# Performance work log

Hardware: AMD Instinct MI355X
Metric: run time of the kernel (lower is better)

Reference implementation:

```python
import jax, jax.numpy as jnp
import numpy as np

# ---- hash-grid config (from module source) ----
L = 16          # n_levels
F = 2           # n_features_per_level
T = 1 << 19     # hashmap size
BASE = 16
SCALE = 1.3819
RES = [int(np.floor(BASE * SCALE ** l)) for l in range(L)]
DENSE = [(r + 1) ** 3 <= T for r in RES]   # levels 0-4 dense, rest hashed
PRIMES = np.array([1, 2654435761, 805459861], dtype=np.uint32)
OFFS = np.array([[i, j, k] for k in (0, 1) for j in (0, 1) for i in (0, 1)], dtype=np.float32)  # [8,3]
OFFS_U = OFFS.astype(np.uint32)


def hash_grid_encode(xyz, table):
    # xyz: [N,3] in [0,1); table: [L,T,F]
    feats = []
    for l in range(L):
        res = RES[l]
        pos = xyz * res                      # [N,3]
        p0f = jnp.floor(pos)
        w = pos - p0f                        # trilinear weights, [N,3]
        p0 = p0f.astype(jnp.uint32)          # [N,3]
        corner = p0[:, None, :] + OFFS_U[None]            # [N,8,3] uint32
        if DENSE[l]:
            s = np.uint32(res + 1)
            idx = corner[..., 0] + corner[..., 1] * s + corner[..., 2] * (s * s)
        else:
            idx = (corner[..., 0] * PRIMES[0]) ^ (corner[..., 1] * PRIMES[1]) ^ (corner[..., 2] * PRIMES[2])
            idx = idx % np.uint32(T)
        # corner weights: prod_d (offs ? w : 1-w)  -> [N,8]
        wts = jnp.prod(jnp.where(OFFS[None].astype(bool), w[:, None, :], 1.0 - w[:, None, :]), axis=-1)
        f = table[l][idx]                    # gather: [N,8,F]
        feats.append(jnp.sum(f * wts[..., None], axis=1))  # [N,F]
    return jnp.concatenate(feats, axis=-1)   # [N, L*F=32]


def sh_deg4(d):
    # d in [-1,1]^3; returns [N,16] real SH basis (tcnn ordering/constants)
    x, y, z = d[:, 0], d[:, 1], d[:, 2]
    x2, y2, z2 = x * x, y * y, z * z
    xy, yz, xz = x * y, y * z, x * z
    return jnp.stack([
        jnp.full_like(x, 0.28209479177387814),
        -0.48860251190291987 * y,
        0.48860251190291987 * z,
        -0.48860251190291987 * x,
        1.0925484305920792 * xy,
        -1.0925484305920792 * yz,
        0.94617469575755997 * z2 - 0.31539156525251999,
        -1.0925484305920792 * xz,
        0.54627421529603959 * (x2 - y2),
        0.59004358992664352 * y * (-3.0 * x2 + y2),
        2.8906114426405538 * xy * z,
        0.45704579946446572 * y * (1.0 - 5.0 * z2),
        0.3731763325901154 * z * (5.0 * z2 - 3.0),
        0.45704579946446572 * x * (1.0 - 5.0 * z2),
        1.4453057213202769 * z * (x2 - y2),
        0.59004358992664352 * x * (-x2 + 3.0 * y2),
    ], axis=-1)


def setup_inputs() -> dict:
    key = jax.random.key(0)
    ks = jax.random.split(key, 8)
    N = 2 ** 21
    xyz = jax.random.uniform(ks[0], (N, 3), dtype=jnp.float32)
    dir = jax.random.uniform(ks[1], (N, 3), dtype=jnp.float32)
    # hash table init per tcnn: uniform in [-1e-4, 1e-4]
    hash_table = jax.random.uniform(ks[2], (L, T, F), dtype=jnp.float32, minval=-1e-4, maxval=1e-4)
    def he(k, fan_in, shape):
        return jax.random.normal(k, shape, dtype=jnp.float32) * np.sqrt(2.0 / fan_in)
    w_sigma1 = he(ks[3], 32, (32, 64))
    w_sigma2 = he(ks[4], 64, (64, 17))   # 1 + geo_feat_dim(16)
    w_rgb1 = he(ks[5], 32, (32, 64))     # 16 (SH) + 16 (geo)
    w_rgb2 = he(ks[6], 64, (64, 64))
    w_rgb3 = he(ks[7], 64, (64, 3))
    return {"xyz": xyz, "dir": dir, "hash_table": hash_table,
            "w_sigma1": w_sigma1, "w_sigma2": w_sigma2,
            "w_rgb1": w_rgb1, "w_rgb2": w_rgb2, "w_rgb3": w_rgb3}


def reference(xyz, dir, hash_table, w_sigma1, w_sigma2, w_rgb1, w_rgb2, w_rgb3):
    xyz_flat = xyz.reshape(-1, 3)
    dir_flat = dir.reshape(-1, 3)
    enc = hash_grid_encode(xyz_flat, hash_table)                 # [N,32]
    h = jax.nn.relu(enc @ w_sigma1)
    geometry = h @ w_sigma2                                       # [N,17]
    sigma, geo_feat = geometry[..., :1], geometry[..., 1:]
    dir_enc = sh_deg4(dir_flat * 2.0 - 1.0)                       # [N,16]
    rgb_in = jnp.concatenate([dir_enc, geo_feat], axis=-1)        # [N,32]
    h = jax.nn.relu(rgb_in @ w_rgb1)
    h = jax.nn.relu(h @ w_rgb2)
    rgb = h @ w_rgb3                                              # [N,3]
    rgb_unflat = rgb.reshape(xyz.shape)
    sigma_unflat = sigma.reshape(xyz.shape[:-1] + (1,))
    return jax.nn.sigmoid(rgb_unflat), jax.nn.relu(sigma_unflat)
```

## Files before the change

### kernel.cpp

```cpp
#include <hip/hip_runtime.h>
#include <hip/hip_bf16.h>
#include <cmath>

#define TBL (1 << 19)

__device__ __forceinline__ float relu_f(float x) { return fmaxf(x, 0.0f); }

__device__ __forceinline__ unsigned short f2bf(float x) {
    union { float f; unsigned u; } v; v.f = x;
    const unsigned r = v.u + 0x7FFFu + ((v.u >> 16) & 1u);
    return (unsigned short)(r >> 16);
}

typedef __attribute__((ext_vector_type(8))) short short8;
typedef __attribute__((ext_vector_type(4))) float floatx4;

#define RES_LIST {16, 22, 30, 42, 58, 80, 111, 153, 212, 294, 406, 561, 775, 1072, 1481, 2047}

__global__ __launch_bounds__(256, 8)
void encode_sched(const float* __restrict__ xyz,
                  const float* __restrict__ table,
                  unsigned* __restrict__ ws_enc,
                  int n)
{
    constexpr unsigned RES[16] = RES_LIST;
    constexpr int LEVORD[16] = {5, 0, 6, 1, 7, 2, 8, 3, 9, 4, 10, 11, 12, 13, 14, 15};

    const int xcd      = (int)(blockIdx.x & 7u);
    const unsigned g   = blockIdx.x >> 3;
    const unsigned upb = (unsigned)(n >> 11);
    const int unit     = (int)(g / upb);
    const int slot     = (int)(g % upb);
    const int level    = LEVORD[unit & 15];
    const int i        = xcd * (n >> 3) + slot * 256 + (int)threadIdx.x;
    if (i >= n) return;

    const float px_ = __builtin_nontemporal_load(xyz + 3 * (size_t)i + 0);
    const float py_ = __builtin_nontemporal_load(xyz + 3 * (size_t)i + 1);
    const float pz_ = __builtin_nontemporal_load(xyz + 3 * (size_t)i + 2);

    const unsigned res = RES[level];
    const float fr = (float)res;
    const float posx = px_ * fr, posy = py_ * fr, posz = pz_ * fr;
    const float fx = floorf(posx), fy = floorf(posy), fz = floorf(posz);
    const float wx = posx - fx, wy = posy - fy, wz = posz - fz;
    const unsigned x0 = (unsigned)fx, y0 = (unsigned)fy, z0 = (unsigned)fz;
    const float* tb = table + (size_t)level * (TBL * 2);

    float a0 = 0.0f, a1 = 0.0f;
    const float wx1 = wx, wx0 = 1.0f - wx;

    if (level < 5) {
        const unsigned s = res + 1u;
        const unsigned s2 = s * s;
        const unsigned base = x0 + y0 * s + z0 * s2;
#pragma unroll
        for (int c = 0; c < 4; ++c) {
            const unsigned dy = c & 1, dz = c >> 1;
            const unsigned idx = base + dy * s + dz * s2;
            const float wyz = (dy ? wy : 1.0f - wy) * (dz ? wz : 1.0f - wz);
            const float w0 = wyz * wx0, w1 = wyz * wx1;
            float e0x, e0y, e1x, e1y;
            if (!(idx & 1u)) {
                const float4 f = *reinterpret_cast<const float4*>(tb + 2u * idx);
                e0x = f.x; e0y = f.y; e1x = f.z; e1y = f.w;
            } else {
                const float2 f0 = *reinterpret_cast<const float2*>(tb + 2u * idx);
                const float2 f1 = *reinterpret_cast<const float2*>(tb + 2u * idx + 2u);
                e0x = f0.x; e0y = f0.y; e1x = f1.x; e1y = f1.y;
            }
            a0 = fmaf(e0x, w0, fmaf(e1x, w1, a0));
            a1 = fmaf(e0y, w0, fmaf(e1y, w1, a1));
        }
    } else {
#pragma unroll
        for (int c = 0; c < 4; ++c) {
            const unsigned dy = c & 1, dz = c >> 1;
            const unsigned hh = (y0 + dy) * 2654435761u ^ (z0 + dz) * 805459861u;
            const float wyz = (dy ? wy : 1.0f - wy) * (dz ? wz : 1.0f - wz);
            const float w0 = wyz * wx0, w1 = wyz * wx1;
            const unsigned i0 = (x0 ^ hh) & (unsigned)(TBL - 1);
            if (!(x0 & 1u)) {
                const float4 f = *reinterpret_cast<const float4*>(tb + 2u * (i0 & ~1u));
                const bool hi = (i0 & 1u) != 0u;
                const float e0x = hi ? f.z : f.x, e0y = hi ? f.w : f.y;
                const float e1x = hi ? f.x : f.z, e1y = hi ? f.y : f.w;
                a0 = fmaf(e0x, w0, fmaf(e1x, w1, a0));
                a1 = fmaf(e0y, w0, fmaf(e1y, w1, a1));
            } else {
                const unsigned i1 = ((x0 + 1u) ^ hh) & (unsigned)(TBL - 1);
                const float2 f0 = *reinterpret_cast<const float2*>(tb + 2u * i0);
                const float2 f1 = *reinterpret_cast<const float2*>(tb + 2u * i1);
                a0 = fmaf(f0.x, w0, fmaf(f1.x, w1, a0));
                a1 = fmaf(f0.y, w0, fmaf(f1.y, w1, a1));
            }
        }
    }

    const unsigned pack = (unsigned)f2bf(a0) | ((unsigned)f2bf(a1) << 16);
    __builtin_nontemporal_store(pack, ws_enc + ((size_t)level * n + i));
}

__global__ __launch_bounds__(256, 4)
void mlp_mfma(const unsigned* __restrict__ ws_enc,
              const float* __restrict__ dirv,
              const float* __restrict__ ws1,
              const float* __restrict__ ws2,
              const float* __restrict__ wr1,
              const float* __restrict__ wr2,
              const float* __restrict__ wr3,
              float* __restrict__ out,
              int n)
{
    __shared__ alignas(16) unsigned short s_w[13184];
    __shared__ alignas(16) unsigned short s_act[4 * 16 * 72];
    __shared__ alignas(16) float          s_geo[4 * 16 * 20];

    const int tid = threadIdx.x;

    for (int e = tid; e < 13184; e += 256) s_w[e] = 0;
    __syncthreads();
    for (int e = tid; e < 2048; e += 256) { const int k = e >> 6, j = e & 63; s_w[0     + j * 40 + k] = f2bf(ws1[e]); }
    for (int e = tid; e < 1088; e += 256) { const int k = e / 17, j = e % 17; s_w[2560  + j * 72 + k] = f2bf(ws2[e]); }
    for (int e = tid; e < 2048; e += 256) { const int k = e >> 6, j = e & 63; s_w[4864  + j * 40 + k] = f2bf(wr1[e]); }
    for (int e = tid; e < 4096; e += 256) { const int k = e >> 6, j = e & 63; s_w[7424  + j * 72 + k] = f2bf(wr2[e]); }
    for (int e = tid; e < 192;  e += 256) { const int k = e / 3,  j = e % 3;  s_w[12032 + j * 72 + k] = f2bf(wr3[e]); }
    __syncthreads();

    const int wave = tid >> 6;
    const int lane = tid & 63;
    const int q    = lane >> 4;
    const int mr   = lane & 15;
    unsigned short* hb = s_act + wave * (16 * 72);
    float*          gb = s_geo + wave * (16 * 20);
    const int base = blockIdx.x * 1024 + wave * 256;
    if (base >= n) return;

    const int pt0 = base + mr;
    unsigned e0 = ws_enc[(size_t)(q * 4 + 0) * n + pt0];
    unsigned e1 = ws_enc[(size_t)(q * 4 + 1) * n + pt0];
    unsigned e2 = ws_enc[(size_t)(q * 4 + 2) * n + pt0];
    unsigned e3 = ws_enc[(size_t)(q * 4 + 3) * n + pt0];
    float dv0 = dirv[3 * (size_t)pt0 + 0];
    float dv1 = dirv[3 * (size_t)pt0 + 1];
    float dv2 = dirv[3 * (size_t)pt0 + 2];

#pragma unroll 1
    for (int mt = 0; mt < 16; ++mt) {
        unsigned f0 = 0, f1 = 0, f2 = 0, f3 = 0;
        float c0 = 0.f, c1 = 0.f, c2 = 0.f;
        if (mt < 15) {
            const int ptn = pt0 + (mt + 1) * 16;
            f0 = ws_enc[(size_t)(q * 4 + 0) * n + ptn];
            f1 = ws_enc[(size_t)(q * 4 + 1) * n + ptn];
            f2 = ws_enc[(size_t)(q * 4 + 2) * n + ptn];
            f3 = ws_enc[(size_t)(q * 4 + 3) * n + ptn];
            c0 = dirv[3 * (size_t)ptn + 0];
            c1 = dirv[3 * (size_t)ptn + 1];
            c2 = dirv[3 * (size_t)ptn + 2];
        }

        short8 aenc;
        aenc[0] = (short)(e0 & 0xFFFFu); aenc[1] = (short)(e0 >> 16);
        aenc[2] = (short)(e1 & 0xFFFFu); aenc[3] = (short)(e1 >> 16);
        aenc[4] = (short)(e2 & 0xFFFFu); aenc[5] = (short)(e2 >> 16);
        aenc[6] = (short)(e3 & 0xFFFFu); aenc[7] = (short)(e3 >> 16);

#pragma unroll
        for (int nc = 0; nc < 4; ++nc) {
            const short8 b = *reinterpret_cast<const short8*>(s_w + 0 + (nc * 16 + mr) * 40 + q * 8);
            floatx4 acc = {0.f, 0.f, 0.f, 0.f};
            acc = __builtin_amdgcn_mfma_f32_16x16x32_bf16(aenc, b, acc, 0, 0, 0);
#pragma unroll
            for (int r = 0; r < 4; ++r)
                hb[(q * 4 + r) * 72 + nc * 16 + mr] = f2bf(fmaxf(acc[r], 0.f));
        }
        __builtin_amdgcn_wave_barrier();

        {
            const short8 a0 = *reinterpret_cast<const short8*>(hb + mr * 72 + 0  + q * 8);
            const short8 a1 = *reinterpret_cast<const short8*>(hb + mr * 72 + 32 + q * 8);
            floatx4 acc0 = {0.f, 0.f, 0.f, 0.f};
            floatx4 acc1 = {0.f, 0.f, 0.f, 0.f};
            {
                const short8 b0 = *reinterpret_cast<const short8*>(s_w + 2560 + mr * 72 + 0  + q * 8);
                const short8 b1 = *reinterpret_cast<const short8*>(s_w + 2560 + mr * 72 + 32 + q * 8);
                acc0 = __builtin_amdgcn_mfma_f32_16x16x32_bf16(a0, b0, acc0, 0, 0, 0);
                acc0 = __builtin_amdgcn_mfma_f32_16x16x32_bf16(a1, b1, acc0, 0, 0, 0);
            }
            {
                const short8 b0 = *reinterpret_cast<const short8*>(s_w + 2560 + (16 + mr) * 72 + 0  + q * 8);
                const short8 b1 = *reinterpret_cast<const short8*>(s_w + 2560 + (16 + mr) * 72 + 32 + q * 8);
                acc1 = __builtin_amdgcn_mfma_f32_16x16x32_bf16(a0, b0, acc1, 0, 0, 0);
                acc1 = __builtin_amdgcn_mfma_f32_16x16x32_bf16(a1, b1, acc1, 0, 0, 0);
            }
#pragma unroll
            for (int r = 0; r < 4; ++r) gb[(q * 4 + r) * 20 + mr + 3] = acc0[r];
            if (mr == 0) {
#pragma unroll
                for (int r = 0; r < 4; ++r) gb[(q * 4 + r) * 20 + 19] = acc1[r];
            }
        }
        __builtin_amdgcn_wave_barrier();

        if (lane < 16)
            out[3 * (size_t)n + (size_t)(base + mt * 16 + lane)] = fmaxf(gb[lane * 20 + 3], 0.f);

        const float dx = dv0 * 2.0f - 1.0f;
        const float dy = dv1 * 2.0f - 1.0f;
        const float dz = dv2 * 2.0f - 1.0f;
        const float x2 = dx * dx, y2 = dy * dy, z2 = dz * dz;
        const float xy = dx * dy, yz = dy * dz, xz = dx * dz;
        float sh[16];
        sh[0]  = 0.28209479177387814f;
        sh[1]  = -0.48860251190291987f * dy;
        sh[2]  = 0.48860251190291987f * dz;
        sh[3]  = -0.48860251190291987f * dx;
        sh[4]  = 1.0925484305920792f * xy;
        sh[5]  = -1.0925484305920792f * yz;
        sh[6]  = 0.94617469575756f * z2 - 0.31539156525252f;
        sh[7]  = -1.0925484305920792f * xz;
        sh[8]  = 0.5462742152960396f * (x2 - y2);
        sh[9]  = 0.5900435899266435f * dy * (-3.0f * x2 + y2);
        sh[10] = 2.890611442640554f * xy * dz;
        sh[11] = 0.4570457994644657f * dy * (1.0f - 5.0f * z2);
        sh[12] = 0.3731763325901154f * dz * (5.0f * z2 - 3.0f);
        sh[13] = 0.4570457994644657f * dx * (1.0f - 5.0f * z2);
        sh[14] = 1.445305721320277f * dz * (x2 - y2);
        sh[15] = 0.5900435899266435f * dx * (-x2 + 3.0f * y2);

        short8 ar;
        if (q < 2) {
#pragma unroll
            for (int j = 0; j < 8; ++j) ar[j] = (short)f2bf(sh[q * 8 + j]);
        } else {
            const floatx4 g0 = *reinterpret_cast<const floatx4*>(gb + mr * 20 + 4 + (q - 2) * 8);
            const floatx4 g1 = *reinterpret_cast<const floatx4*>(gb + mr * 20 + 8 + (q - 2) * 8);
#pragma unroll
            for (int j = 0; j < 4; ++j) { ar[j] = (short)f2bf(g0[j]); ar[4 + j] = (short)f2bf(g1[j]); }
        }

#pragma unroll
        for (int nc = 0; nc < 4; ++nc) {
            const short8 b = *reinterpret_cast<const short8*>(s_w + 4864 + (nc * 16 + mr) * 40 + q * 8);
            floatx4 acc = {0.f, 0.f, 0.f, 0.f};
            acc = __builtin_amdgcn_mfma_f32_16x16x32_bf16(ar, b, acc, 0, 0, 0);
#pragma unroll
            for (int r = 0; r < 4; ++r)
                hb[(q * 4 + r) * 72 + nc * 16 + mr] = f2bf(fmaxf(acc[r], 0.f));
        }
        __builtin_amdgcn_wave_barrier();

        {
            const short8 a0 = *reinterpret_cast<const short8*>(hb + mr * 72 + 0  + q * 8);
            const short8 a1 = *reinterpret_cast<const short8*>(hb + mr * 72 + 32 + q * 8);
            __builtin_amdgcn_wave_barrier();
#pragma unroll
            for (int nc = 0; nc < 4; ++nc) {
                const short8 b0 = *reinterpret_cast<const short8*>(s_w + 7424 + (nc * 16 + mr) * 72 + 0  + q * 8);
                const short8 b1 = *reinterpret_cast<const short8*>(s_w + 7424 + (nc * 16 + mr) * 72 + 32 + q * 8);
                floatx4 acc = {0.f, 0.f, 0.f, 0.f};
                acc = __builtin_amdgcn_mfma_f32_16x16x32_bf16(a0, b0, acc, 0, 0, 0);
                acc = __builtin_amdgcn_mfma_f32_16x16x32_bf16(a1, b1, acc, 0, 0, 0);
#pragma unroll
                for (int r = 0; r < 4; ++r)
                    hb[(q * 4 + r) * 72 + nc * 16 + mr] = f2bf(fmaxf(acc[r], 0.f));
            }
        }
        __builtin_amdgcn_wave_barrier();

        {
            const short8 a0 = *reinterpret_cast<const short8*>(hb + mr * 72 + 0  + q * 8);
            const short8 a1 = *reinterpret_cast<const short8*>(hb + mr * 72 + 32 + q * 8);
            const short8 b0 = *reinterpret_cast<const short8*>(s_w + 12032 + mr * 72 + 0  + q * 8);
            const short8 b1 = *reinterpret_cast<const short8*>(s_w + 12032 + mr * 72 + 32 + q * 8);
            floatx4 acc = {0.f, 0.f, 0.f, 0.f};
            acc = __builtin_amdgcn_mfma_f32_16x16x32_bf16(a0, b0, acc, 0, 0, 0);
            acc = __builtin_amdgcn_mfma_f32_16x16x32_bf16(a1, b1, acc, 0, 0, 0);
            if (mr < 3) {
#pragma unroll
                for (int r = 0; r < 4; ++r) {
                    const int p = base + mt * 16 + q * 4 + r;
                    out[3 * (size_t)p + mr] = 1.0f / (1.0f + __expf(-acc[r]));
                }
            }
        }
        __builtin_amdgcn_wave_barrier();

        e0 = f0; e1 = f1; e2 = f2; e3 = f3;
        dv0 = c0; dv1 = c1; dv2 = c2;
    }
}

__global__ __launch_bounds__(256, 4)
void nerf_fused(const float* __restrict__ xyz,
                const float* __restrict__ dirv,
                const float* __restrict__ table,
                const float* __restrict__ ws1,
                const float* __restrict__ ws2,
                const float* __restrict__ wr1,
                const float* __restrict__ wr2,
                const float* __restrict__ wr3,
                float* __restrict__ out,
                int n)
{
    constexpr unsigned RES[16] = RES_LIST;

    const int i = blockIdx.x * 256 + threadIdx.x;
    if (i >= n) return;

    const float px_ = xyz[3 * (size_t)i + 0];
    const float py_ = xyz[3 * (size_t)i + 1];
    const float pz_ = xyz[3 * (size_t)i + 2];

    float enc[32];
#pragma unroll
    for (int l = 0; l < 16; ++l) {
        const unsigned res = RES[l];
        const float fr = (float)res;
        const float posx = px_ * fr, posy = py_ * fr, posz = pz_ * fr;
        const float fx = floorf(posx), fy = floorf(posy), fz = floorf(posz);
        const float wx = posx - fx, wy = posy - fy, wz = posz - fz;
        const unsigned x0 = (unsigned)fx, y0 = (unsigned)fy, z0 = (unsigned)fz;
        const float* tb = table + (size_t)l * (TBL * 2);
        float a0 = 0.0f, a1 = 0.0f;
#pragma unroll
        for (int c = 0; c < 8; ++c) {
            const unsigned cx = x0 + (c & 1);
            const unsigned cy = y0 + ((c >> 1) & 1);
            const unsigned cz = z0 + ((c >> 2) & 1);
            unsigned idx;
            if (l < 5) {
                const unsigned s = res + 1u;
                idx = cx + cy * s + cz * (s * s);
            } else {
                idx = (cx * 1u) ^ (cy * 2654435761u) ^ (cz * 805459861u);
                idx &= (unsigned)(TBL - 1);
            }
            const float w = ((c & 1) ? wx : 1.0f - wx) *
                            ((c & 2) ? wy : 1.0f - wy) *
                            ((c & 4) ? wz : 1.0f - wz);
            const float2 f = *reinterpret_cast<const float2*>(tb + 2u * idx);
            a0 = fmaf(f.x, w, a0);
            a1 = fmaf(f.y, w, a1);
        }
        enc[2 * l + 0] = a0;
        enc[2 * l + 1] = a1;
    }

    float h[64];
#pragma unroll
    for (int j = 0; j < 64; ++j) h[j] = 0.0f;
#pragma unroll
    for (int k = 0; k < 32; ++k) {
        const float e = enc[k];
#pragma unroll
        for (int j = 0; j < 64; ++j) h[j] = fmaf(e, ws1[k * 64 + j], h[j]);
    }
#pragma unroll
    for (int j = 0; j < 64; ++j) h[j] = relu_f(h[j]);

    float geo[17];
#pragma unroll
    for (int j = 0; j < 17; ++j) geo[j] = 0.0f;
#pragma unroll
    for (int k = 0; k < 64; ++k) {
        const float e = h[k];
#pragma unroll
        for (int j = 0; j < 17; ++j) geo[j] = fmaf(e, ws2[k * 17 + j], geo[j]);
    }
    out[3 * (size_t)n + (size_t)i] = relu_f(geo[0]);

    const float dx = dirv[3 * (size_t)i + 0] * 2.0f - 1.0f;
    const float dy = dirv[3 * (size_t)i + 1] * 2.0f - 1.0f;
    const float dz = dirv[3 * (size_t)i + 2] * 2.0f - 1.0f;
    const float x2 = dx * dx, y2 = dy * dy, z2 = dz * dz;
    const float xy = dx * dy, yz = dy * dz, xz = dx * dz;

    float sh[16];
    sh[0]  = 0.28209479177387814f;
    sh[1]  = -0.48860251190291987f * dy;
    sh[2]  = 0.48860251190291987f * dz;
    sh[3]  = -0.48860251190291987f * dx;
    sh[4]  = 1.0925484305920792f * xy;
    sh[5]  = -1.0925484305920792f * yz;
    sh[6]  = 0.94617469575756f * z2 - 0.31539156525252f;
    sh[7]  = -1.0925484305920792f * xz;
    sh[8]  = 0.5462742152960396f * (x2 - y2);
    sh[9]  = 0.5900435899266435f * dy * (-3.0f * x2 + y2);
    sh[10] = 2.890611442640554f * xy * dz;
    sh[11] = 0.4570457994644657f * dy * (1.0f - 5.0f * z2);
    sh[12] = 0.3731763325901154f * dz * (5.0f * z2 - 3.0f);
    sh[13] = 0.4570457994644657f * dx * (1.0f - 5.0f * z2);
    sh[14] = 1.445305721320277f * dz * (x2 - y2);
    sh[15] = 0.5900435899266435f * dx * (-x2 + 3.0f * y2);

    float g[64];
#pragma unroll
    for (int j = 0; j < 64; ++j) g[j] = 0.0f;
#pragma unroll
    for (int k = 0; k < 16; ++k) {
        const float e = sh[k];
#pragma unroll
        for (int j = 0; j < 64; ++j) g[j] = fmaf(e, wr1[k * 64 + j], g[j]);
    }
#pragma unroll
    for (int k = 16; k < 32; ++k) {
        const float e = geo[k - 15];
#pragma unroll
        for (int j = 0; j < 64; ++j) g[j] = fmaf(e, wr1[k * 64 + j], g[j]);
    }
#pragma unroll
    for (int j = 0; j < 64; ++j) g[j] = relu_f(g[j]);

    float r0 = 0.0f, r1 = 0.0f, r2 = 0.0f;
#pragma unroll
    for (int half = 0; half < 2; ++half) {
        const int j0 = half * 32;
        float g2h[32];
#pragma unroll
        for (int j = 0; j < 32; ++j) g2h[j] = 0.0f;
#pragma unroll
        for (int k = 0; k < 64; ++k) {
            const float e = g[k];
#pragma unroll
            for (int j = 0; j < 32; ++j) g2h[j] = fmaf(e, wr2[k * 64 + j0 + j], g2h[j]);
        }
#pragma unroll
        for (int j = 0; j < 32; ++j) {
            const float e = relu_f(g2h[j]);
            r0 = fmaf(e, wr3[(j0 + j) * 3 + 0], r0);
            r1 = fmaf(e, wr3[(j0 + j) * 3 + 1], r1);
            r2 = fmaf(e, wr3[(j0 + j) * 3 + 2], r2);
        }
    }

    out[3 * (size_t)i + 0] = 1.0f / (1.0f + __expf(-r0));
    out[3 * (size_t)i + 1] = 1.0f / (1.0f + __expf(-r1));
    out[3 * (size_t)i + 2] = 1.0f / (1.0f + __expf(-r2));
}

extern "C" void kernel_launch(void* const* d_in, const int* in_sizes, int n_in,
                              void* d_out, int out_size, void* d_ws, size_t ws_size,
                              hipStream_t stream)
{
    const float* xyz   = (const float*)d_in[0];
    const float* dirv  = (const float*)d_in[1];
    const float* table = (const float*)d_in[2];
    const float* ws1   = (const float*)d_in[3];
    const float* ws2   = (const float*)d_in[4];
    const float* wr1   = (const float*)d_in[5];
    const float* wr2   = (const float*)d_in[6];
    const float* wr3   = (const float*)d_in[7];
    float* out = (float*)d_out;

    const int n = in_sizes[0] / 3;
    dim3 block(256);

    const size_t enc_bytes = (size_t)n * 16 * sizeof(unsigned);
    if (ws_size >= enc_bytes && n >= 2048 && (n & 2047) == 0) {
        unsigned* ws_enc = (unsigned*)d_ws;
        dim3 grid_enc(8u * 16u * (unsigned)(n >> 11));
        dim3 grid_mlp((unsigned)(n >> 10));
        hipLaunchKernelGGL(encode_sched, grid_enc, block, 0, stream,
                           xyz, table, ws_enc, n);
        hipLaunchKernelGGL(mlp_mfma, grid_mlp, block, 0, stream,
                           ws_enc, dirv, ws1, ws2, wr1, wr2, wr3, out, n);
    } else {
        dim3 grid_mlp((n + 255) / 256);
        hipLaunchKernelGGL(nerf_fused, grid_mlp, block, 0, stream,
                           xyz, dirv, table, ws1, ws2, wr1, wr2, wr3, out, n);
    }
}
```

Before: 966.3 us.

## Keep MLP activations in registers via transposed MFMA and permuted weights

```diff
diff --git a/kernel.cpp b/kernel.cpp
--- a/kernel.cpp
+++ b/kernel.cpp
@@ -14,6 +14,10 @@
 
 typedef __attribute__((ext_vector_type(8))) short short8;
 typedef __attribute__((ext_vector_type(4))) float floatx4;
+
+__device__ __forceinline__ int sperm(int k) {
+    return ((k >> 5) << 5) | (((k >> 2) & 3) << 3) | (((k >> 4) & 1) << 2) | (k & 3);
+}
 
 #define RES_LIST {16, 22, 30, 42, 58, 80, 111, 153, 212, 294, 406, 561, 775, 1072, 1481, 2047}
 
@@ -101,7 +105,7 @@
     __builtin_nontemporal_store(pack, ws_enc + ((size_t)level * n + i));
 }
 
-__global__ __launch_bounds__(256, 4)
+__global__ __launch_bounds__(256)
 void mlp_mfma(const unsigned* __restrict__ ws_enc,
               const float* __restrict__ dirv,
               const float* __restrict__ ws1,
@@ -112,29 +116,33 @@
               float* __restrict__ out,
               int n)
 {
-    __shared__ alignas(16) unsigned short s_w[13184];
-    __shared__ alignas(16) unsigned short s_act[4 * 16 * 72];
-    __shared__ alignas(16) float          s_geo[4 * 16 * 20];
+    __shared__ alignas(16) unsigned short s_w[12032];
+    __shared__ alignas(8)  unsigned short s_geo[4][16 * 20];
 
     const int tid = threadIdx.x;
 
-    for (int e = tid; e < 13184; e += 256) s_w[e] = 0;
+    for (int e = tid; e < 12032; e += 256) s_w[e] = 0;
     __syncthreads();
-    for (int e = tid; e < 2048; e += 256) { const int k = e >> 6, j = e & 63; s_w[0     + j * 40 + k] = f2bf(ws1[e]); }
-    for (int e = tid; e < 1088; e += 256) { const int k = e / 17, j = e % 17; s_w[2560  + j * 72 + k] = f2bf(ws2[e]); }
-    for (int e = tid; e < 2048; e += 256) { const int k = e >> 6, j = e & 63; s_w[4864  + j * 40 + k] = f2bf(wr1[e]); }
-    for (int e = tid; e < 4096; e += 256) { const int k = e >> 6, j = e & 63; s_w[7424  + j * 72 + k] = f2bf(wr2[e]); }
-    for (int e = tid; e < 192;  e += 256) { const int k = e / 3,  j = e % 3;  s_w[12032 + j * 72 + k] = f2bf(wr3[e]); }
+    for (int e = tid; e < 2048; e += 256) { const int k = e >> 6, j = e & 63; s_w[0    + j * 40 + k] = f2bf(ws1[e]); }
+    for (int e = tid; e < 1088; e += 256) { const int k = e / 17, j = e % 17; s_w[2560 + j * 72 + sperm(k)] = f2bf(ws2[e]); }
+    for (int e = tid; e < 2048; e += 256) { const int k = e >> 6, j = e & 63; s_w[4864 + j * 40 + k] = f2bf(wr1[e]); }
+    for (int e = tid; e < 4096; e += 256) { const int k = e >> 6, j = e & 63; s_w[7424 + j * 72 + sperm(k)] = f2bf(wr2[e]); }
     __syncthreads();
 
     const int wave = tid >> 6;
     const int lane = tid & 63;
     const int q    = lane >> 4;
     const int mr   = lane & 15;
-    unsigned short* hb = s_act + wave * (16 * 72);
-    float*          gb = s_geo + wave * (16 * 20);
+    unsigned short* gb = s_geo[wave];
     const int base = blockIdx.x * 1024 + wave * 256;
     if (base >= n) return;
+
+    float w3v[4][3];
+#pragma unroll
+    for (int t = 0; t < 4; ++t)
+#pragma unroll
+        for (int c = 0; c < 3; ++c)
+            w3v[t][c] = wr3[(t * 16 + mr) * 3 + c];
 
     const int pt0 = base + mr;
     unsigned e0 = ws_enc[(size_t)(q * 4 + 0) * n + pt0];
@@ -145,12 +153,16 @@
     float dv1 = dirv[3 * (size_t)pt0 + 1];
     float dv2 = dirv[3 * (size_t)pt0 + 2];
 
+    union U8 { unsigned u[4]; short8 s; };
+
 #pragma unroll 1
-    for (int mt = 0; mt < 16; ++mt) {
+    for (int it = 0; it < 16; ++it) {
+        const int pb = base + it * 16;
+
         unsigned f0 = 0, f1 = 0, f2 = 0, f3 = 0;
         float c0 = 0.f, c1 = 0.f, c2 = 0.f;
-        if (mt < 15) {
-            const int ptn = pt0 + (mt + 1) * 16;
+        if (it < 15) {
+            const int ptn = pt0 + (it + 1) * 16;
             f0 = ws_enc[(size_t)(q * 4 + 0) * n + ptn];
             f1 = ws_enc[(size_t)(q * 4 + 1) * n + ptn];
             f2 = ws_enc[(size_t)(q * 4 + 2) * n + ptn];
@@ -160,51 +172,55 @@
             c2 = dirv[3 * (size_t)ptn + 2];
         }
 
-        short8 aenc;
-        aenc[0] = (short)(e0 & 0xFFFFu); aenc[1] = (short)(e0 >> 16);
-        aenc[2] = (short)(e1 & 0xFFFFu); aenc[3] = (short)(e1 >> 16);
-        aenc[4] = (short)(e2 & 0xFFFFu); aenc[5] = (short)(e2 >> 16);
-        aenc[6] = (short)(e3 & 0xFFFFu); aenc[7] = (short)(e3 >> 16);
-
-#pragma unroll
-        for (int nc = 0; nc < 4; ++nc) {
-            const short8 b = *reinterpret_cast<const short8*>(s_w + 0 + (nc * 16 + mr) * 40 + q * 8);
+        U8 be; be.u[0] = e0; be.u[1] = e1; be.u[2] = e2; be.u[3] = e3;
+        const short8 benc = be.s;
+
+        floatx4 h4[4];
+#pragma unroll
+        for (int t = 0; t < 4; ++t) {
+            const short8 a = *reinterpret_cast<const short8*>(s_w + 0 + (t * 16 + mr) * 40 + q * 8);
             floatx4 acc = {0.f, 0.f, 0.f, 0.f};
-            acc = __builtin_amdgcn_mfma_f32_16x16x32_bf16(aenc, b, acc, 0, 0, 0);
+            h4[t] = __builtin_amdgcn_mfma_f32_16x16x32_bf16(a, benc, acc, 0, 0, 0);
+        }
+
+        short8 A0, A1;
+#pragma unroll
+        for (int j = 0; j < 4; ++j) {
+            A0[j]     = (short)f2bf(fmaxf(h4[0][j], 0.f));
+            A0[4 + j] = (short)f2bf(fmaxf(h4[1][j], 0.f));
+            A1[j]     = (short)f2bf(fmaxf(h4[2][j], 0.f));
+            A1[4 + j] = (short)f2bf(fmaxf(h4[3][j], 0.f));
+        }
+
+        floatx4 g0acc = {0.f, 0.f, 0.f, 0.f};
+        floatx4 g1acc = {0.f, 0.f, 0.f, 0.f};
+        {
+            const short8 b00 = *reinterpret_cast<const short8*>(s_w + 2560 + mr * 72 + 0  + q * 8);
+            const short8 b01 = *reinterpret_cast<const short8*>(s_w + 2560 + mr * 72 + 32 + q * 8);
+            g0acc = __builtin_amdgcn_mfma_f32_16x16x32_bf16(A0, b00, g0acc, 0, 0, 0);
+            g0acc = __builtin_amdgcn_mfma_f32_16x16x32_bf16(A1, b01, g0acc, 0, 0, 0);
+            const short8 b10 = *reinterpret_cast<const short8*>(s_w + 2560 + (16 + mr) * 72 + 0  + q * 8);
+            const short8 b11 = *reinterpret_cast<const short8*>(s_w + 2560 + (16 + mr) * 72 + 32 + q * 8);
+            g1acc = __builtin_amdgcn_mfma_f32_16x16x32_bf16(A0, b10, g1acc, 0, 0, 0);
+            g1acc = __builtin_amdgcn_mfma_f32_16x16x32_bf16(A1, b11, g1acc, 0, 0, 0);
+        }
+
+        if (mr == 0) {
 #pragma unroll
             for (int r = 0; r < 4; ++r)
-                hb[(q * 4 + r) * 72 + nc * 16 + mr] = f2bf(fmaxf(acc[r], 0.f));
+                out[3 * (size_t)n + (size_t)(pb + q * 4 + r)] = fmaxf(g0acc[r], 0.f);
+        }
+
+        if (mr != 0) {
+#pragma unroll
+            for (int r = 0; r < 4; ++r)
+                gb[(q * 4 + r) * 20 + (mr - 1)] = f2bf(g0acc[r]);
+        } else {
+#pragma unroll
+            for (int r = 0; r < 4; ++r)
+                gb[(q * 4 + r) * 20 + 15] = f2bf(g1acc[r]);
         }
         __builtin_amdgcn_wave_barrier();
-
-        {
-            const short8 a0 = *reinterpret_cast<const short8*>(hb + mr * 72 + 0  + q * 8);
-            const short8 a1 = *reinterpret_cast<const short8*>(hb + mr * 72 + 32 + q * 8);
-            floatx4 acc0 = {0.f, 0.f, 0.f, 0.f};
-            floatx4 acc1 = {0.f, 0.f, 0.f, 0.f};
-            {
-                const short8 b0 = *reinterpret_cast<const short8*>(s_w + 2560 + mr * 72 + 0  + q * 8);
-                const short8 b1 = *reinterpret_cast<const short8*>(s_w + 2560 + mr * 72 + 32 + q * 8);
-                acc0 = __builtin_amdgcn_mfma_f32_16x16x32_bf16(a0, b0, acc0, 0, 0, 0);
-                acc0 = __builtin_amdgcn_mfma_f32_16x16x32_bf16(a1, b1, acc0, 0, 0, 0);
-            }
-            {
-                const short8 b0 = *reinterpret_cast<const short8*>(s_w + 2560 + (16 + mr) * 72 + 0  + q * 8);
-                const short8 b1 = *reinterpret_cast<const short8*>(s_w + 2560 + (16 + mr) * 72 + 32 + q * 8);
-                acc1 = __builtin_amdgcn_mfma_f32_16x16x32_bf16(a0, b0, acc1, 0, 0, 0);
-                acc1 = __builtin_amdgcn_mfma_f32_16x16x32_bf16(a1, b1, acc1, 0, 0, 0);
-            }
-#pragma unroll
-            for (int r = 0; r < 4; ++r) gb[(q * 4 + r) * 20 + mr + 3] = acc0[r];
-            if (mr == 0) {
-#pragma unroll
-                for (int r = 0; r < 4; ++r) gb[(q * 4 + r) * 20 + 19] = acc1[r];
-            }
-        }
-        __builtin_amdgcn_wave_barrier();
-
-        if (lane < 16)
-            out[3 * (size_t)n + (size_t)(base + mt * 16 + lane)] = fmaxf(gb[lane * 20 + 3], 0.f);
 
         const float dx = dv0 * 2.0f - 1.0f;
         const float dy = dv1 * 2.0f - 1.0f;
@@ -229,61 +245,81 @@
         sh[14] = 1.445305721320277f * dz * (x2 - y2);
         sh[15] = 0.5900435899266435f * dx * (-x2 + 3.0f * y2);
 
-        short8 ar;
-        if (q < 2) {
-#pragma unroll
-            for (int j = 0; j < 8; ++j) ar[j] = (short)f2bf(sh[q * 8 + j]);
-        } else {
-            const floatx4 g0 = *reinterpret_cast<const floatx4*>(gb + mr * 20 + 4 + (q - 2) * 8);
-            const floatx4 g1 = *reinterpret_cast<const floatx4*>(gb + mr * 20 + 8 + (q - 2) * 8);
-#pragma unroll
-            for (int j = 0; j < 4; ++j) { ar[j] = (short)f2bf(g0[j]); ar[4 + j] = (short)f2bf(g1[j]); }
-        }
-
-#pragma unroll
-        for (int nc = 0; nc < 4; ++nc) {
-            const short8 b = *reinterpret_cast<const short8*>(s_w + 4864 + (nc * 16 + mr) * 40 + q * 8);
+        const int sb = (q & 1) * 8;
+        unsigned shw0 = (unsigned)f2bf(sh[sb + 0]) | ((unsigned)f2bf(sh[sb + 1]) << 16);
+        unsigned shw1 = (unsigned)f2bf(sh[sb + 2]) | ((unsigned)f2bf(sh[sb + 3]) << 16);
+        unsigned shw2 = (unsigned)f2bf(sh[sb + 4]) | ((unsigned)f2bf(sh[sb + 5]) << 16);
+        unsigned shw3 = (unsigned)f2bf(sh[sb + 6]) | ((unsigned)f2bf(sh[sb + 7]) << 16);
+        const unsigned* gp = reinterpret_cast<const unsigned*>(gb + mr * 20 + sb);
+        U8 br;
+        br.u[0] = (q < 2) ? shw0 : gp[0];
+        br.u[1] = (q < 2) ? shw1 : gp[1];
+        br.u[2] = (q < 2) ? shw2 : gp[2];
+        br.u[3] = (q < 2) ? shw3 : gp[3];
+        const short8 brgb = br.s;
+
+        floatx4 gg[4];
+#pragma unroll
+        for (int t = 0; t < 4; ++t) {
+            const short8 a = *reinterpret_cast<const short8*>(s_w + 4864 + (t * 16 + mr) * 40 + q * 8);
             floatx4 acc = {0.f, 0.f, 0.f, 0.f};
-            acc = __builtin_amdgcn_mfma_f32_16x16x32_bf16(ar, b, acc, 0, 0, 0);
+            gg[t] = __builtin_amdgcn_mfma_f32_16x16x32_bf16(a, brgb, acc, 0, 0, 0);
+        }
+
+        short8 Ag0, Ag1;
+#pragma unroll
+        for (int j = 0; j < 4; ++j) {
+            Ag0[j]     = (short)f2bf(fmaxf(gg[0][j], 0.f));
+            Ag0[4 + j] = (short)f2bf(fmaxf(gg[1][j], 0.f));
+            Ag1[j]     = (short)f2bf(fmaxf(gg[2][j], 0.f));
+            Ag1[4 + j] = (short)f2bf(fmaxf(gg[3][j], 0.f));
+        }
+
+        floatx4 g2[4];
+#pragma unroll
+        for (int t = 0; t < 4; ++t) {
+            const short8 b0 = *reinterpret_cast<const short8*>(s_w + 7424 + (t * 16 + mr) * 72 + 0  + q * 8);
+            const short8 b1 = *reinterpret_cast<const short8*>(s_w + 7424 + (t * 16 + mr) * 72 + 32 + q * 8);
+            floatx4 acc = {0.f, 0.f, 0.f, 0.f};
+            acc = __builtin_amdgcn_mfma_f32_16x16x32_bf16(Ag0, b0, acc, 0, 0, 0);
+            acc = __builtin_amdgcn_mfma_f32_16x16x32_bf16(Ag1, b1, acc, 0, 0, 0);
+            g2[t] = acc;
+        }
+
+        float part[3][4];
+#pragma unroll
+        for (int c = 0; c < 3; ++c)
+#pragma unroll
+            for (int r = 0; r < 4; ++r) part[c][r] = 0.f;
+#pragma unroll
+        for (int t = 0; t < 4; ++t) {
+#pragma unroll
+            for (int r = 0; r < 4; ++r) {
+                const float v = fmaxf(g2[t][r], 0.f);
+#pragma unroll
+                for (int c = 0; c < 3; ++c) part[c][r] = fmaf(v, w3v[t][c], part[c][r]);
+            }
+        }
+#pragma unroll
+        for (int m = 1; m < 16; m <<= 1) {
+#pragma unroll
+            for (int c = 0; c < 3; ++c)
+#pragma unroll
+                for (int r = 0; r < 4; ++r)
+                    part[c][r] += __shfl_xor(part[c][r], m);
+        }
+        if (mr == 0) {
 #pragma unroll
             for (int r = 0; r < 4; ++r)
-                hb[(q * 4 + r) * 72 + nc * 16 + mr] = f2bf(fmaxf(acc[r], 0.f));
-        }
-        __builtin_amdgcn_wave_barrier();
-
-        {
-            const short8 a0 = *reinterpret_cast<const short8*>(hb + mr * 72 + 0  + q * 8);
-            const short8 a1 = *reinterpret_cast<const short8*>(hb + mr * 72 + 32 + q * 8);
-            __builtin_amdgcn_wave_barrier();
-#pragma unroll
-            for (int nc = 0; nc < 4; ++nc) {
-                const short8 b0 = *reinterpret_cast<const short8*>(s_w + 7424 + (nc * 16 + mr) * 72 + 0  + q * 8);
-                const short8 b1 = *reinterpret_cast<const short8*>(s_w + 7424 + (nc * 16 + mr) * 72 + 32 + q * 8);
-                floatx4 acc = {0.f, 0.f, 0.f, 0.f};
-                acc = __builtin_amdgcn_mfma_f32_16x16x32_bf16(a0, b0, acc, 0, 0, 0);
-                acc = __builtin_amdgcn_mfma_f32_16x16x32_bf16(a1, b1, acc, 0, 0, 0);
-#pragma unroll
-                for (int r = 0; r < 4; ++r)
-                    hb[(q * 4 + r) * 72 + nc * 16 + mr] = f2bf(fmaxf(acc[r], 0.f));
-            }
-        }
-        __builtin_amdgcn_wave_barrier();
-
-        {
-            const short8 a0 = *reinterpret_cast<const short8*>(hb + mr * 72 + 0  + q * 8);
-            const short8 a1 = *reinterpret_cast<const short8*>(hb + mr * 72 + 32 + q * 8);
-            const short8 b0 = *reinterpret_cast<const short8*>(s_w + 12032 + mr * 72 + 0  + q * 8);
-            const short8 b1 = *reinterpret_cast<const short8*>(s_w + 12032 + mr * 72 + 32 + q * 8);
-            floatx4 acc = {0.f, 0.f, 0.f, 0.f};
-            acc = __builtin_amdgcn_mfma_f32_16x16x32_bf16(a0, b0, acc, 0, 0, 0);
-            acc = __builtin_amdgcn_mfma_f32_16x16x32_bf16(a1, b1, acc, 0, 0, 0);
-            if (mr < 3) {
-#pragma unroll
-                for (int r = 0; r < 4; ++r) {
-                    const int p = base + mt * 16 + q * 4 + r;
-                    out[3 * (size_t)p + mr] = 1.0f / (1.0f + __expf(-acc[r]));
-                }
-            }
+                out[3 * (size_t)(pb + q * 4 + r) + 0] = 1.0f / (1.0f + __expf(-part[0][r]));
+        } else if (mr == 1) {
+#pragma unroll
+            for (int r = 0; r < 4; ++r)
+                out[3 * (size_t)(pb + q * 4 + r) + 1] = 1.0f / (1.0f + __expf(-part[1][r]));
+        } else if (mr == 2) {
+#pragma unroll
+            for (int r = 0; r < 4; ++r)
+                out[3 * (size_t)(pb + q * 4 + r) + 2] = 1.0f / (1.0f + __expf(-part[2][r]));
         }
         __builtin_amdgcn_wave_barrier();
 
```

New measurement: 997.2 us. 1.03x slower.
